# Kernel tuning notes

Hardware: AMD Instinct MI355X
Metric: run time of the kernel (lower is better)

Reference implementation:

```python
import jax, jax.numpy as jnp
import numpy as np

C = 256; GC = 32; G = C // GC; K = 3; S = 1; NEW = 2; PAD = (K - 1) // 2
IN1 = C * K * 2 + C * K * K // 32          # 1608
OUT1 = G * NEW * NEW * K * K // 4          # 72
OUT2 = G * NEW * NEW * K * K               # 288
B = 8; H = 56; W = 56


def setup_inputs():
    key = jax.random.key(0)
    k0, k1, k2 = jax.random.split(key, 3)
    inputs = jax.random.normal(k0, (B, C, H, W), jnp.float32)
    W1 = jax.random.normal(k1, (OUT1, IN1), jnp.float32) * np.float32(1.0 / np.sqrt(IN1))
    b1 = jnp.zeros((OUT1,), jnp.float32)
    W2 = jax.random.normal(k2, (OUT2, OUT1), jnp.float32) * np.float32(1.0 / np.sqrt(OUT1))
    b2 = jnp.zeros((OUT2,), jnp.float32)
    return {"inputs": inputs, "W1": W1, "b1": b1, "W2": W2, "b2": b2}


def _unfold(x, h, w):
    # torch.nn.Unfold(K, 1, PAD, S): patches of shape (B, C, K, K, h, w)
    xp = jnp.pad(x, ((0, 0), (0, 0), (PAD, PAD), (PAD, PAD)))
    cols = [xp[:, :, di:di + (h - 1) * S + 1:S, dj:dj + (w - 1) * S + 1:S]
            for di in range(K) for dj in range(K)]  # fixed K*K=9 slices
    return jnp.stack(cols, axis=2).reshape(x.shape[0], x.shape[1], K, K, h, w)


def reference(inputs, W1, b1, W2, b2):
    b, c, Hh, Ww = inputs.shape
    h = (Hh + 2 * PAD - K) // S + 1
    w = (Ww + 2 * PAD - K) // S + 1
    # (B, G, GC, K, K, h, w)
    x = _unfold(inputs, h, w).reshape(b, G, GC, K, K, h, w)
    # three max-pooled descriptors over different axes
    x1 = x.reshape(b, G, -1, GC // 32, K, K, h, w).max(axis=2).reshape(b, -1, h, w)  # (B, C*K*K//32, h, w)
    x2 = x.max(axis=3).reshape(b, -1, h, w)  # (B, C*K, h, w)
    x3 = x.max(axis=4).reshape(b, -1, h, w)  # (B, C*K, h, w)
    feat = jnp.concatenate([x1, x2, x3], axis=1)  # (B, IN1, h, w)
    # two biased 1x1 convs (ConvModule with no norm/act)
    y = jnp.einsum('bchw,oc->bohw', feat, W1) + b1[None, :, None, None]
    y = jnp.einsum('bchw,oc->bohw', y, W2) + b2[None, :, None, None]
    # softmax over the K*K kernel-window dim
    wgt = jax.nn.softmax(y.reshape(b, G, K * K, NEW * NEW, h, w), axis=2)
    # softmax-weighted local aggregation: sum over kernel window
    agg = jnp.einsum('bgckhw,bgknhw->bgcnhw', x.reshape(b, G, GC, K * K, h, w), wgt)
    # fold with non-overlapping (NEW, NEW) blocks == block upsampling reshape
    return agg.reshape(b, C, NEW, NEW, h, w).transpose(0, 1, 4, 2, 5, 3).reshape(b, C, h * NEW, w * NEW)
```

## Files before the change

kernel.cpp:

```cpp
#include <hip/hip_runtime.h>

#define CC   256
#define HH   56
#define WWID 56
#define KIN1 1608
#define KP1  1632
#define NO1  72
#define NO2  288
#define PPB  14
#define H2   112
#define W2D  112

typedef unsigned short u16;
typedef unsigned int   u32;
typedef __attribute__((ext_vector_type(8))) short v8s;
typedef __attribute__((ext_vector_type(4))) float v4f;

#define W1BF_ELEMS (80 * KP1)
#define W2BF_OFF_B 262144

#define LDS_TOTAL 32768
#define OFF_A 0
#define OFF_B 21504
#define OFF_C 29696

#define SWZ(row) (((row) & 7) << 3)

__device__ __forceinline__ u16 f2b(float x) {
  u32 u = __float_as_uint(x);
  u = (u + 0x7FFFu + ((u >> 16) & 1u)) >> 16;
  return (u16)u;
}

__global__ void kConvW(const float* __restrict__ W1, const float* __restrict__ W2,
                       u16* __restrict__ w1bf, u16* __restrict__ w2bf) {
  int idx = blockIdx.x * 256 + threadIdx.x;
  if (idx < W1BF_ELEMS) {
    int m = idx / KP1, k = idx - m * KP1;
    float v = 0.f;
    if (m < NO1) {
      int orig = -1;
      if (k < 768)                 orig = 72 + (k & 255) * 3 + (k >> 8);
      else if (k < 1536)           orig = 840 + (k & 255) * 3 + ((k - 768) >> 8);
      else if ((k - 1536) < NO1)   orig = k - 1536;
      if (orig >= 0) v = W1[m * KIN1 + orig];
    }
    w1bf[idx] = f2b(v);
  } else {
    int i2 = idx - W1BF_ELEMS;
    if (i2 < NO2 * 96) {
      int m = i2 / 96, k = i2 - m * 96;
      w2bf[i2] = (k < NO1) ? f2b(W2[m * NO1 + k]) : (u16)0;
    }
  }
}

__global__ __launch_bounds__(256, 4)
void kFused(const float* __restrict__ in, const u16* __restrict__ w1bf,
            const float* __restrict__ b1, const u16* __restrict__ w2bf,
            const float* __restrict__ b2, float* __restrict__ out) {
  __shared__ __align__(16) char lds[LDS_TOTAL];
  u16*   rowmaxT = (u16*)(lds + OFF_A);
  u16*   colmaxT = (u16*)(lds + OFF_B);
  u16*   x1T     = (u16*)(lds + OFF_C);
  float* partA   = (float*)(lds + OFF_A);
  float* y2L     = (float*)(lds + OFF_A);
  float* tile    = (float*)(lds + OFF_A);

  const int t  = threadIdx.x;
  const int L  = blockIdx.x + 4 * (blockIdx.y + 56 * blockIdx.z);
  const int jq = L >> 3;
  const int jt = jq & 3, i = jq >> 2, b = L & 7;
  const int c  = t;
  const int g  = c >> 5;
  const int gc = c & 31;
  const int w  = t >> 6, lane = t & 63;
  const int ml = lane & 15, quad = lane >> 4;

  {
    u32* xu = (u32*)x1T;
    if (t < 132) {
#pragma unroll
      for (int rp2 = 0; rp2 < 2; ++rp2) {
        int idx = 2 * t + rp2;
        if (idx < 192) {
          int row = idx / 12;
          xu[(row * 48 + 36 + (idx - row * 12)) ^ ((row & 7) << 2)] = 0u;
        } else {
          int e = idx - 192, row = 14 + e / 36;
          xu[(row * 48 + (e % 36)) ^ ((row & 7) << 2)] = 0u;
        }
      }
    }
  }

  const float* rowbase0 = in + ((size_t)b * CC + c) * (HH * WWID);
  u32 win_p[3][8];
  float colmax[16];
#pragma unroll
  for (int k = 0; k < 16; ++k) colmax[k] = -3.0e38f;

#pragma unroll
  for (int r = 0; r < 3; ++r) {
    const int row = i - 1 + r;
    float sc[16];
    if (row < 0 || row >= HH) {
#pragma unroll
      for (int k = 0; k < 16; ++k) sc[k] = 0.f;
    } else {
      const float* rp = rowbase0 + row * WWID;
      float l[20];
      if (jt == 0) {
        const float4 a0 = *(const float4*)(rp), a1 = *(const float4*)(rp + 4),
                     a2 = *(const float4*)(rp + 8), a3 = *(const float4*)(rp + 12);
        l[0]=a0.x;l[1]=a0.y;l[2]=a0.z;l[3]=a0.w; l[4]=a1.x;l[5]=a1.y;l[6]=a1.z;l[7]=a1.w;
        l[8]=a2.x;l[9]=a2.y;l[10]=a2.z;l[11]=a2.w; l[12]=a3.x;l[13]=a3.y;l[14]=a3.z;l[15]=a3.w;
        sc[0] = 0.f;
#pragma unroll
        for (int k = 1; k < 16; ++k) sc[k] = l[k - 1];
      } else if (jt == 3) {
        const float* q = rp + 40;
        const float4 a0 = *(const float4*)(q), a1 = *(const float4*)(q + 4),
                     a2 = *(const float4*)(q + 8), a3 = *(const float4*)(q + 12);
        l[0]=a0.x;l[1]=a0.y;l[2]=a0.z;l[3]=a0.w; l[4]=a1.x;l[5]=a1.y;l[6]=a1.z;l[7]=a1.w;
        l[8]=a2.x;l[9]=a2.y;l[10]=a2.z;l[11]=a2.w; l[12]=a3.x;l[13]=a3.y;l[14]=a3.z;l[15]=a3.w;
#pragma unroll
        for (int k = 0; k < 15; ++k) sc[k] = l[k + 1];
        sc[15] = 0.f;
      } else {
        const float* q = rp + ((jt == 1) ? 12 : 24);
        const float4 a0 = *(const float4*)(q), a1 = *(const float4*)(q + 4),
                     a2 = *(const float4*)(q + 8), a3 = *(const float4*)(q + 12),
                     a4 = *(const float4*)(q + 16);
        l[0]=a0.x;l[1]=a0.y;l[2]=a0.z;l[3]=a0.w; l[4]=a1.x;l[5]=a1.y;l[6]=a1.z;l[7]=a1.w;
        l[8]=a2.x;l[9]=a2.y;l[10]=a2.z;l[11]=a2.w; l[12]=a3.x;l[13]=a3.y;l[14]=a3.z;l[15]=a3.w;
        l[16]=a4.x;l[17]=a4.y;l[18]=a4.z;l[19]=a4.w;
        if (jt == 1) {
#pragma unroll
          for (int k = 0; k < 16; ++k) sc[k] = l[k + 1];
        } else {
#pragma unroll
          for (int k = 0; k < 16; ++k) sc[k] = l[k + 3];
        }
      }
    }
#pragma unroll
    for (int k = 0; k < 16; ++k) colmax[k] = fmaxf(colmax[k], sc[k]);
#pragma unroll
    for (int n = 0; n < 14; ++n)
      rowmaxT[(n * 768 + r * 256 + c) ^ SWZ(n)] =
          f2b(fmaxf(fmaxf(sc[n], sc[n + 1]), sc[n + 2]));
#pragma unroll
    for (int col = 0; col < 16; ++col) {
      float m = sc[col];
      m = fmaxf(m, __shfl_xor(m, 1));
      m = fmaxf(m, __shfl_xor(m, 2));
      m = fmaxf(m, __shfl_xor(m, 4));
      m = fmaxf(m, __shfl_xor(m, 8));
      m = fmaxf(m, __shfl_xor(m, 16));
      if (gc == col) {
        u16 mv = f2b(m);
#pragma unroll
        for (int kj = 0; kj < 3; ++kj) {
          const int n = col - kj;
          if (n >= 0 && n < 14)
            x1T[(n * 96 + g * 9 + r * 3 + kj) ^ SWZ(n)] = mv;
        }
      }
    }
#pragma unroll
    for (int k = 0; k < 8; ++k)
      win_p[r][k] = (u32)f2b(sc[2 * k]) | ((u32)f2b(sc[2 * k + 1]) << 16);
  }
#pragma unroll
  for (int col = 0; col < 16; ++col)
    colmaxT[(col * 256 + c) ^ SWZ(col)] = f2b(colmax[col]);
  __syncthreads();

  v4f acc[5];
#pragma unroll
  for (int mt = 0; mt < 5; ++mt) acc[mt] = (v4f){0.f, 0.f, 0.f, 0.f};
  const int ks0 = w * 13, ks1 = (w == 3) ? 51 : ks0 + 13;

  auto loadB = [&](int ks) -> v8s {
    if (ks < 24) {
      int kj = ks >> 3, c0 = (ks & 7) * 32, rowi = ml + kj;
      return *(v8s*)&colmaxT[(rowi * 256 + c0 + quad * 8) ^ SWZ(rowi)];
    } else if (ks < 48) {
      return *(v8s*)&rowmaxT[(ml * 768 + (ks - 24) * 32 + quad * 8) ^ SWZ(ml)];
    } else {
      return *(v8s*)&x1T[(ml * 96 + (ks - 48) * 32 + quad * 8) ^ SWZ(ml)];
    }
  };

  {
    v8s bf_c = loadB(ks0);
    v8s af_c[5];
    {
      const int k0 = ks0 * 32 + quad * 8;
#pragma unroll
      for (int mt = 0; mt < 5; ++mt)
        af_c[mt] = *(const v8s*)&w1bf[(mt * 16 + ml) * KP1 + k0];
    }
    for (int ks = ks0; ks < ks1; ++ks) {
      v8s bf_n, af_n[5];
      if (ks + 1 < ks1) {
        bf_n = loadB(ks + 1);
        const int k0n = (ks + 1) * 32 + quad * 8;
#pragma unroll
        for (int mt = 0; mt < 5; ++mt)
          af_n[mt] = *(const v8s*)&w1bf[(mt * 16 + ml) * KP1 + k0n];
      }
#pragma unroll
      for (int mt = 0; mt < 5; ++mt)
        acc[mt] = __builtin_amdgcn_mfma_f32_16x16x32_bf16(af_c[mt], bf_c, acc[mt], 0, 0, 0);
      if (ks + 1 < ks1) {
        bf_c = bf_n;
#pragma unroll
        for (int mt = 0; mt < 5; ++mt) af_c[mt] = af_n[mt];
      }
    }
  }
  __syncthreads();

#pragma unroll
  for (int mt = 0; mt < 5; ++mt)
    *(v4f*)&partA[((w * 5 + mt) * 16 + ml) * 16 + quad * 4] = acc[mt];
  __syncthreads();

  u16* y1b = x1T;
#pragma unroll
  for (int it = 0; it < 4; ++it) {
    int e = t + it * 256;
    if (e < NO1 * PPB) {
      int m = e / PPB, n = e - m * PPB;
      float s = b1[m];
#pragma unroll
      for (int ww = 0; ww < 4; ++ww)
        s += partA[((ww * 5 + (m >> 4)) * 16 + n) * 16 + (m & 15)];
      y1b[(n * 96 + m) ^ SWZ(n)] = f2b(s);
    }
  }
  __syncthreads();

  {
    v8s bfr[3];
#pragma unroll
    for (int ks = 0; ks < 3; ++ks)
      bfr[ks] = *(v8s*)&y1b[(ml * 96 + ks * 32 + quad * 8) ^ SWZ(ml)];
    const int mt0 = (w < 2) ? 5 * w : 10 + 4 * (w - 2);
    const int mtn = (w < 2) ? 5 : 4;
    for (int mi = 0; mi < mtn; ++mi) {
      const int mt = mt0 + mi;
      v4f a2 = (v4f){0.f, 0.f, 0.f, 0.f};
#pragma unroll
      for (int ks = 0; ks < 3; ++ks) {
        v8s af = *(const v8s*)&w2bf[(mt * 16 + ml) * 96 + ks * 32 + quad * 8];
        a2 = __builtin_amdgcn_mfma_f32_16x16x32_bf16(af, bfr[ks], a2, 0, 0, 0);
      }
      const int o0 = mt * 16 + quad * 4;
      const float4 bv = *(const float4*)(b2 + o0);
      a2[0] += bv.x; a2[1] += bv.y; a2[2] += bv.z; a2[3] += bv.w;
      *(v4f*)&y2L[ml * 296 + o0] = a2;
    }
  }
  __syncthreads();

#pragma unroll
  for (int it = 0; it < 2; ++it) {
    int s2 = t + it * 256;
    if (s2 < 448) {
      int gg = s2 / 56, rem = s2 - gg * 56, nn = rem / PPB, n = rem - nn * PPB;
      float* bp = &y2L[n * 296 + gg * 36 + nn];
      float v9[9], m = -1e30f;
#pragma unroll
      for (int k = 0; k < 9; ++k) { v9[k] = bp[k * 4]; m = fmaxf(m, v9[k]); }
      float sum = 0.f;
#pragma unroll
      for (int k = 0; k < 9; ++k) { v9[k] = __expf(v9[k] - m); sum += v9[k]; }
      float inv = 1.f / sum;
#pragma unroll
      for (int k = 0; k < 9; ++k) bp[k * 4] = v9[k] * inv;
    }
  }
  __syncthreads();

  float a0s[14], a1s[14], a2s[14], a3s[14];
#pragma unroll
  for (int n = 0; n < 14; ++n) {
    const v4f* wp = (const v4f*)&y2L[n * 296 + g * 36];
    float a0 = 0.f, a1 = 0.f, a2v = 0.f, a3 = 0.f;
#pragma unroll
    for (int r = 0; r < 3; ++r) {
      float x0, x1, x2v;
      if ((n & 1) == 0) {
        u32 ua = win_p[r][n >> 1], ub = win_p[r][(n >> 1) + 1];
        x0  = __uint_as_float(ua << 16);
        x1  = __uint_as_float(ua & 0xffff0000u);
        x2v = __uint_as_float(ub << 16);
      } else {
        u32 ua = win_p[r][n >> 1], ub = win_p[r][(n >> 1) + 1];
        x0  = __uint_as_float(ua & 0xffff0000u);
        x1  = __uint_as_float(ub << 16);
        x2v = __uint_as_float(ub & 0xffff0000u);
      }
#pragma unroll
      for (int kj = 0; kj < 3; ++kj) {
        v4f wv = wp[r * 3 + kj];
        float x = (kj == 0) ? x0 : (kj == 1) ? x1 : x2v;
        a0  = fmaf(x, wv[0], a0);
        a1  = fmaf(x, wv[1], a1);
        a2v = fmaf(x, wv[2], a2v);
        a3  = fmaf(x, wv[3], a3);
      }
    }
    a0s[n] = a0; a1s[n] = a1; a2s[n] = a2v; a3s[n] = a3;
  }
  __syncthreads();

  const int cl = c & 63;
  for (int ch = 0; ch < 4; ++ch) {
    if ((c >> 6) == ch) {
#pragma unroll
      for (int n = 0; n < 14; ++n) {
        float2 lo2; lo2.x = a0s[n]; lo2.y = a1s[n];
        float2 hi2; hi2.x = a2s[n]; hi2.y = a3s[n];
        *(float2*)&tile[cl * 60 + 2 * n] = lo2;
        *(float2*)&tile[cl * 60 + 28 + 2 * n] = hi2;
      }
    }
    __syncthreads();
#pragma unroll
    for (int it = 0; it < 4; ++it) {
      int f = t + it * 256;
      if (f < 896) {
        int rr = f / 7, xi = f - rr * 7;
        int cg = ch * 64 + (rr >> 1), di = rr & 1;
        v4f val = *(v4f*)&tile[(rr >> 1) * 60 + di * 28 + xi * 4];
        *(v4f*)&out[((size_t)(b * CC + cg) * H2 + (size_t)(2 * i + di)) * W2D
                    + 28 * jt + xi * 4] = val;
      }
    }
    __syncthreads();
  }
}

extern "C" void kernel_launch(void* const* d_in, const int* in_sizes, int n_in,
                              void* d_out, int out_size, void* d_ws, size_t ws_size,
                              hipStream_t stream) {
  const float* in = (const float*)d_in[0];
  const float* W1 = (const float*)d_in[1];
  const float* b1 = (const float*)d_in[2];
  const float* W2 = (const float*)d_in[3];
  const float* b2 = (const float*)d_in[4];
  float* out = (float*)d_out;

  u16* w1bf = (u16*)d_ws;
  u16* w2bf = (u16*)((char*)d_ws + W2BF_OFF_B);

  const int B = in_sizes[0] / (CC * HH * WWID);

  kConvW<<<dim3((W1BF_ELEMS + NO2 * 96 + 255) / 256), 256, 0, stream>>>(W1, W2, w1bf, w2bf);
  dim3 grid(WWID / PPB, HH, B);
  kFused<<<grid, 256, 0, stream>>>(in, w1bf, b1, w2bf, b2, out);
}
```

Measured before the change: 208.6 us.

## Split first conv by output rows per wave and write output directly from registers

The first 1x1 conv now assigns output-row tiles to waves, each running the full K range, instead of splitting K across waves. This removes the partial-sum LDS buffer, its reduction pass and two barriers, and adds bias and a bf16 store straight to a new dedicated y1 LDS region. The final aggregation now writes float4 rows directly to global memory per thread, dropping the LDS transpose tile and its eight barriers. In exchange, wave 0 does twice the MFMA work of the other waves, which creates imbalance, and the direct per-channel global stores may be less coalesced.

```diff
diff --git a/kernel.cpp b/kernel.cpp
--- a/kernel.cpp
+++ b/kernel.cpp
@@ -15,14 +15,16 @@
 typedef unsigned int   u32;
 typedef __attribute__((ext_vector_type(8))) short v8s;
 typedef __attribute__((ext_vector_type(4))) float v4f;
+typedef __attribute__((ext_vector_type(4))) unsigned short us4;
 
 #define W1BF_ELEMS (80 * KP1)
 #define W2BF_OFF_B 262144
 
-#define LDS_TOTAL 32768
+#define LDS_TOTAL 35840
 #define OFF_A 0
 #define OFF_B 21504
 #define OFF_C 29696
+#define OFF_D 32768
 
 #define SWZ(row) (((row) & 7) << 3)
 
@@ -63,9 +65,8 @@
   u16*   rowmaxT = (u16*)(lds + OFF_A);
   u16*   colmaxT = (u16*)(lds + OFF_B);
   u16*   x1T     = (u16*)(lds + OFF_C);
-  float* partA   = (float*)(lds + OFF_A);
+  u16*   y1b     = (u16*)(lds + OFF_D);
   float* y2L     = (float*)(lds + OFF_A);
-  float* tile    = (float*)(lds + OFF_A);
 
   const int t  = threadIdx.x;
   const int L  = blockIdx.x + 4 * (blockIdx.y + 56 * blockIdx.z);
@@ -79,17 +80,21 @@
 
   {
     u32* xu = (u32*)x1T;
+    u32* yu = (u32*)y1b;
     if (t < 132) {
 #pragma unroll
       for (int rp2 = 0; rp2 < 2; ++rp2) {
         int idx = 2 * t + rp2;
+        int off;
         if (idx < 192) {
           int row = idx / 12;
-          xu[(row * 48 + 36 + (idx - row * 12)) ^ ((row & 7) << 2)] = 0u;
+          off = (row * 48 + 36 + (idx - row * 12)) ^ ((row & 7) << 2);
         } else {
           int e = idx - 192, row = 14 + e / 36;
-          xu[(row * 48 + (e % 36)) ^ ((row & 7) << 2)] = 0u;
-        }
+          off = (row * 48 + (e % 36)) ^ ((row & 7) << 2);
+        }
+        xu[off] = 0u;
+        yu[off] = 0u;
       }
     }
   }
@@ -177,11 +182,6 @@
     colmaxT[(col * 256 + c) ^ SWZ(col)] = f2b(colmax[col]);
   __syncthreads();
 
-  v4f acc[5];
-#pragma unroll
-  for (int mt = 0; mt < 5; ++mt) acc[mt] = (v4f){0.f, 0.f, 0.f, 0.f};
-  const int ks0 = w * 13, ks1 = (w == 3) ? 51 : ks0 + 13;
-
   auto loadB = [&](int ks) -> v8s {
     if (ks < 24) {
       int kj = ks >> 3, c0 = (ks & 7) * 32, rowi = ml + kj;
@@ -194,51 +194,47 @@
   };
 
   {
-    v8s bf_c = loadB(ks0);
-    v8s af_c[5];
-    {
-      const int k0 = ks0 * 32 + quad * 8;
-#pragma unroll
-      for (int mt = 0; mt < 5; ++mt)
-        af_c[mt] = *(const v8s*)&w1bf[(mt * 16 + ml) * KP1 + k0];
-    }
-    for (int ks = ks0; ks < ks1; ++ks) {
-      v8s bf_n, af_n[5];
-      if (ks + 1 < ks1) {
-        bf_n = loadB(ks + 1);
-        const int k0n = (ks + 1) * 32 + quad * 8;
-#pragma unroll
-        for (int mt = 0; mt < 5; ++mt)
-          af_n[mt] = *(const v8s*)&w1bf[(mt * 16 + ml) * KP1 + k0n];
-      }
-#pragma unroll
-      for (int mt = 0; mt < 5; ++mt)
-        acc[mt] = __builtin_amdgcn_mfma_f32_16x16x32_bf16(af_c[mt], bf_c, acc[mt], 0, 0, 0);
-      if (ks + 1 < ks1) {
-        bf_c = bf_n;
-#pragma unroll
-        for (int mt = 0; mt < 5; ++mt) af_c[mt] = af_n[mt];
-      }
-    }
-  }
-  __syncthreads();
-
-#pragma unroll
-  for (int mt = 0; mt < 5; ++mt)
-    *(v4f*)&partA[((w * 5 + mt) * 16 + ml) * 16 + quad * 4] = acc[mt];
-  __syncthreads();
-
-  u16* y1b = x1T;
-#pragma unroll
-  for (int it = 0; it < 4; ++it) {
-    int e = t + it * 256;
-    if (e < NO1 * PPB) {
-      int m = e / PPB, n = e - m * PPB;
-      float s = b1[m];
-#pragma unroll
-      for (int ww = 0; ww < 4; ++ww)
-        s += partA[((ww * 5 + (m >> 4)) * 16 + n) * 16 + (m & 15)];
-      y1b[(n * 96 + m) ^ SWZ(n)] = f2b(s);
+    v4f acc0 = (v4f){0.f, 0.f, 0.f, 0.f};
+    const u16* ap0 = w1bf + (w * 16 + ml) * KP1 + quad * 8;
+    if (w == 0) {
+      v4f acc1 = (v4f){0.f, 0.f, 0.f, 0.f};
+      const u16* ap1 = w1bf + (64 + ml) * KP1 + quad * 8;
+#pragma unroll
+      for (int ks = 0; ks < 51; ++ks) {
+        v8s bf = loadB(ks);
+        v8s a0 = *(const v8s*)(ap0 + ks * 32);
+        v8s a1 = *(const v8s*)(ap1 + ks * 32);
+        acc0 = __builtin_amdgcn_mfma_f32_16x16x32_bf16(a0, bf, acc0, 0, 0, 0);
+        acc1 = __builtin_amdgcn_mfma_f32_16x16x32_bf16(a1, bf, acc1, 0, 0, 0);
+      }
+      if (ml < 14) {
+        const float4 bv0 = *(const float4*)(b1 + quad * 4);
+        us4 h0;
+        h0.x = f2b(acc0[0] + bv0.x); h0.y = f2b(acc0[1] + bv0.y);
+        h0.z = f2b(acc0[2] + bv0.z); h0.w = f2b(acc0[3] + bv0.w);
+        *(us4*)&y1b[(ml * 96 + quad * 4) ^ SWZ(ml)] = h0;
+        if (quad < 2) {
+          const float4 bv1 = *(const float4*)(b1 + 64 + quad * 4);
+          us4 h1;
+          h1.x = f2b(acc1[0] + bv1.x); h1.y = f2b(acc1[1] + bv1.y);
+          h1.z = f2b(acc1[2] + bv1.z); h1.w = f2b(acc1[3] + bv1.w);
+          *(us4*)&y1b[(ml * 96 + 64 + quad * 4) ^ SWZ(ml)] = h1;
+        }
+      }
+    } else {
+#pragma unroll
+      for (int ks = 0; ks < 51; ++ks) {
+        v8s bf = loadB(ks);
+        v8s a0 = *(const v8s*)(ap0 + ks * 32);
+        acc0 = __builtin_amdgcn_mfma_f32_16x16x32_bf16(a0, bf, acc0, 0, 0, 0);
+      }
+      if (ml < 14) {
+        const float4 bv0 = *(const float4*)(b1 + w * 16 + quad * 4);
+        us4 h0;
+        h0.x = f2b(acc0[0] + bv0.x); h0.y = f2b(acc0[1] + bv0.y);
+        h0.z = f2b(acc0[2] + bv0.z); h0.w = f2b(acc0[3] + bv0.w);
+        *(us4*)&y1b[(ml * 96 + w * 16 + quad * 4) ^ SWZ(ml)] = h0;
+      }
     }
   }
   __syncthreads();
@@ -285,63 +281,39 @@
   }
   __syncthreads();
 
-  float a0s[14], a1s[14], a2s[14], a3s[14];
-#pragma unroll
-  for (int n = 0; n < 14; ++n) {
-    const v4f* wp = (const v4f*)&y2L[n * 296 + g * 36];
-    float a0 = 0.f, a1 = 0.f, a2v = 0.f, a3 = 0.f;
-#pragma unroll
-    for (int r = 0; r < 3; ++r) {
-      float x0, x1, x2v;
-      if ((n & 1) == 0) {
-        u32 ua = win_p[r][n >> 1], ub = win_p[r][(n >> 1) + 1];
-        x0  = __uint_as_float(ua << 16);
-        x1  = __uint_as_float(ua & 0xffff0000u);
-        x2v = __uint_as_float(ub << 16);
-      } else {
-        u32 ua = win_p[r][n >> 1], ub = win_p[r][(n >> 1) + 1];
-        x0  = __uint_as_float(ua & 0xffff0000u);
-        x1  = __uint_as_float(ub << 16);
-        x2v = __uint_as_float(ub & 0xffff0000u);
-      }
-#pragma unroll
-      for (int kj = 0; kj < 3; ++kj) {
-        v4f wv = wp[r * 3 + kj];
-        float x = (kj == 0) ? x0 : (kj == 1) ? x1 : x2v;
-        a0  = fmaf(x, wv[0], a0);
-        a1  = fmaf(x, wv[1], a1);
-        a2v = fmaf(x, wv[2], a2v);
-        a3  = fmaf(x, wv[3], a3);
-      }
-    }
-    a0s[n] = a0; a1s[n] = a1; a2s[n] = a2v; a3s[n] = a3;
-  }
-  __syncthreads();
-
-  const int cl = c & 63;
-  for (int ch = 0; ch < 4; ++ch) {
-    if ((c >> 6) == ch) {
-#pragma unroll
-      for (int n = 0; n < 14; ++n) {
-        float2 lo2; lo2.x = a0s[n]; lo2.y = a1s[n];
-        float2 hi2; hi2.x = a2s[n]; hi2.y = a3s[n];
-        *(float2*)&tile[cl * 60 + 2 * n] = lo2;
-        *(float2*)&tile[cl * 60 + 28 + 2 * n] = hi2;
-      }
-    }
-    __syncthreads();
-#pragma unroll
-    for (int it = 0; it < 4; ++it) {
-      int f = t + it * 256;
-      if (f < 896) {
-        int rr = f / 7, xi = f - rr * 7;
-        int cg = ch * 64 + (rr >> 1), di = rr & 1;
-        v4f val = *(v4f*)&tile[(rr >> 1) * 60 + di * 28 + xi * 4];
-        *(v4f*)&out[((size_t)(b * CC + cg) * H2 + (size_t)(2 * i + di)) * W2D
-                    + 28 * jt + xi * 4] = val;
-      }
-    }
-    __syncthreads();
+  {
+    float* orow0 = out + ((size_t)(b * CC + c) * H2 + (size_t)(2 * i)) * W2D + 28 * jt;
+    float* orow1 = orow0 + W2D;
+#pragma unroll
+    for (int x = 0; x < 7; ++x) {
+      const v4f* wp0 = (const v4f*)&y2L[(2 * x) * 296 + g * 36];
+      const v4f* wp1 = (const v4f*)&y2L[(2 * x + 1) * 296 + g * 36];
+      float e0 = 0.f, e1 = 0.f, e2 = 0.f, e3 = 0.f;
+      float o0 = 0.f, o1 = 0.f, o2 = 0.f, o3 = 0.f;
+#pragma unroll
+      for (int r = 0; r < 3; ++r) {
+        u32 ua = win_p[r][x], ub = win_p[r][x + 1];
+        float ex0 = __uint_as_float(ua << 16);
+        float ex1 = __uint_as_float(ua & 0xffff0000u);
+        float ex2 = __uint_as_float(ub << 16);
+        float ox2 = __uint_as_float(ub & 0xffff0000u);
+#pragma unroll
+        for (int kj = 0; kj < 3; ++kj) {
+          v4f wv0 = wp0[r * 3 + kj];
+          v4f wv1 = wp1[r * 3 + kj];
+          float xe = (kj == 0) ? ex0 : (kj == 1) ? ex1 : ex2;
+          float xo = (kj == 0) ? ex1 : (kj == 1) ? ex2 : ox2;
+          e0 = fmaf(xe, wv0[0], e0); e1 = fmaf(xe, wv0[1], e1);
+          e2 = fmaf(xe, wv0[2], e2); e3 = fmaf(xe, wv0[3], e3);
+          o0 = fmaf(xo, wv1[0], o0); o1 = fmaf(xo, wv1[1], o1);
+          o2 = fmaf(xo, wv1[2], o2); o3 = fmaf(xo, wv1[3], o3);
+        }
+      }
+      v4f v0 = (v4f){e0, e1, o0, o1};
+      v4f v1 = (v4f){e2, e3, o2, o3};
+      *(v4f*)(orow0 + 4 * x) = v0;
+      *(v4f*)(orow1 + 4 * x) = v1;
+    }
   }
 }
 
```

After: 215.6 us. 3.4% more time.
